# Kernel optimization log

Measured on AMD Instinct MI355X. Metric: run time of the kernel, lower is better.

Reference implementation:

```python
import jax, jax.numpy as jnp
import numpy as np

E, CIN, COUT, K = 8, 256, 256, 3
STRIDE, PAD, DIL, GROUPS = 1, 1, 1, 1
N, H, W = 32, 56, 56


def setup_inputs() -> dict:
    key = jax.random.key(0)
    k1, k2, k3 = jax.random.split(key, 3)
    x = jax.random.normal(k1, (N, CIN, H, W), jnp.float32)
    # expert weight bank: (E*COUT, CIN//GROUPS, K, K), as in the torch module
    weight = jax.random.normal(k2, (E * COUT, CIN // GROUPS, K, K), jnp.float32) * 0.05
    fc_w = jax.random.normal(k3, (E, CIN), jnp.float32) * 0.02
    fc_b = jnp.zeros((E,), jnp.float32)
    return {"x": x, "weight": weight, "fc_w": fc_w, "fc_b": fc_b}


def reference(x, weight, fc_w, fc_b):
    n = x.shape[0]
    # sigmoid gate from global-avg-pooled features: (n, E)
    gate = jax.nn.sigmoid(x.mean((2, 3)) @ fc_w.T + fc_b)
    # mix expert weights per sample: (n, COUT, CIN//GROUPS, K, K)
    w = (gate @ weight.reshape(E, -1)).reshape(n, COUT, CIN // GROUPS, K, K)

    def conv1(xi, wi):
        # xi: (CIN, H, W), wi: (COUT, CIN//GROUPS, K, K)
        return jax.lax.conv_general_dilated(
            xi[None], wi,
            window_strides=(STRIDE, STRIDE),
            padding=[(PAD, PAD), (PAD, PAD)],
            rhs_dilation=(DIL, DIL),
            feature_group_count=GROUPS,
            dimension_numbers=("NCHW", "OIHW", "NCHW"),
        )[0]

    return jax.vmap(conv1)(x, w)  # (n, COUT, H_out, W_out)
```

## Files before the change

kernel.cpp:

```cpp
#include <hip/hip_runtime.h>
#include <hip/hip_bf16.h>

#define E_    8
#define CIN_  256
#define COUT_ 256
#define NK    9
#define KTOT  2304
#define IMGH  56
#define IMGW  56
#define HW    3136
#define NBATCH 32
#define PADW  58
#define PADHW 3364

typedef __attribute__((ext_vector_type(8))) __bf16 bf16x8;
typedef __attribute__((ext_vector_type(4))) float f32x4;
typedef unsigned int u32;

__device__ __forceinline__ void gld_lds16(const __bf16* g, __bf16* l) {
    __builtin_amdgcn_global_load_lds(
        (const __attribute__((address_space(1))) void*)(g),
        (__attribute__((address_space(3))) void*)(l), 16, 0, 0);
}

__global__ __launch_bounds__(256) void halo_zero_kernel(__bf16* xTp) {
    const int total = NBATCH * 228 * 128;
    u32* p = (u32*)xTp;
    for (int idx = blockIdx.x * 256 + threadIdx.x; idx < total; idx += gridDim.x * 256) {
        const int n  = idx / (228 * 128);
        const int r  = idx - n * (228 * 128);
        const int hp = r >> 7;
        const int cp = r & 127;
        int px;
        if (hp < 58)       px = hp;
        else if (hp < 116) px = 57 * PADW + (hp - 58);
        else if (hp < 172) px = (hp - 116 + 1) * PADW;
        else               px = (hp - 172 + 1) * PADW + 57;
        p[((size_t)(n * PADHW + px)) * 128 + cp] = 0u;
    }
}

__global__ __launch_bounds__(256) void transpose_kernel(const float* __restrict__ x,
                                                        __bf16* __restrict__ xTp,
                                                        float* __restrict__ pooled) {
    __shared__ __bf16 t[64][66];
    const int px0 = blockIdx.x * 64;
    const int c0  = blockIdx.y * 64;
    const int n   = blockIdx.z;
    const int tid = threadIdx.x;
    {
        const int px_l = tid & 63;
        const int cb   = (tid >> 6) * 16;
        #pragma unroll
        for (int i = 0; i < 16; ++i) {
            const int cin_l = cb + i;
            t[cin_l][px_l] =
                (__bf16)x[((size_t)(n * CIN_ + c0 + cin_l)) * HW + px0 + px_l];
        }
    }
    __syncthreads();
    {
        const int cin_l = tid & 63;
        const int pb    = (tid >> 6) * 16;
        float s = 0.f;
        #pragma unroll
        for (int i = 0; i < 16; ++i) {
            const int px = px0 + pb + i;
            const int h  = px / IMGW;
            const int w  = px - h * IMGW;
            const __bf16 v = t[cin_l][pb + i];
            s += (float)v;
            xTp[((size_t)(n * PADHW + (h + 1) * PADW + (w + 1))) * CIN_ + c0 + cin_l] = v;
        }
        atomicAdd(&pooled[n * CIN_ + c0 + cin_l], s);
    }
}

__global__ __launch_bounds__(256) void gate_kernel(const float* __restrict__ pooled,
                                                   const float* __restrict__ fc_w,
                                                   const float* __restrict__ fc_b,
                                                   float* __restrict__ gate) {
    const int t = threadIdx.x;
    const int n = t >> 3, e = t & 7;
    const float* pv = pooled + n * CIN_;
    const float* wv = fc_w + e * CIN_;
    float s = 0.f;
    for (int c = 0; c < CIN_; ++c) s += pv[c] * wv[c];
    s = s * (1.0f / HW) + fc_b[e];
    gate[t] = 1.0f / (1.0f + expf(-s));
}

__global__ __launch_bounds__(256) void mix_kernel(const float* __restrict__ weight,
                                                  const float* __restrict__ gate,
                                                  __bf16* __restrict__ wmix) {
    __shared__ float wstage[KTOT];
    __shared__ __bf16 tlds[KTOT];
    const int cout = blockIdx.x;
    const int tid  = threadIdx.x;
    float wreg[E_][NK];
    for (int e = 0; e < E_; ++e) {
        const float* wp = weight + (size_t)(e * COUT_ + cout) * KTOT;
        #pragma unroll
        for (int i = 0; i < NK; ++i) wstage[tid + i * 256] = wp[tid + i * 256];
        __syncthreads();
        #pragma unroll
        for (int kk = 0; kk < NK; ++kk) wreg[e][kk] = wstage[tid * NK + kk];
        __syncthreads();
    }
    for (int n = 0; n < NBATCH; ++n) {
        float g[E_];
        #pragma unroll
        for (int e = 0; e < E_; ++e) g[e] = gate[n * E_ + e];
        float acc[NK];
        #pragma unroll
        for (int kk = 0; kk < NK; ++kk) acc[kk] = 0.f;
        #pragma unroll
        for (int e = 0; e < E_; ++e)
            #pragma unroll
            for (int kk = 0; kk < NK; ++kk) acc[kk] += g[e] * wreg[e][kk];
        #pragma unroll
        for (int kk = 0; kk < NK; ++kk) tlds[kk * 256 + tid] = (__bf16)acc[kk];
        __syncthreads();
        u32* dst = (u32*)(wmix + ((size_t)(n * COUT_ + cout)) * KTOT);
        const u32* src = (const u32*)tlds;
        #pragma unroll
        for (int j = 0; j < 4; ++j) dst[tid + j * 256] = src[tid + j * 256];
        if (tid < 128) dst[tid + 1024] = src[tid + 1024];
        __syncthreads();
    }
}

#define BM 256
#define BN 224

__global__ __launch_bounds__(512) void conv_kernel(const __bf16* __restrict__ xTp,
                                                   const __bf16* __restrict__ wmix,
                                                   float* __restrict__ out) {
    __shared__ __attribute__((aligned(16))) __bf16 At[2][BM * 64];
    __shared__ __attribute__((aligned(16))) __bf16 Bt[2][BN * 64];

    const int bid = blockIdx.x;
    const int swz = (bid & 7) * 56 + (bid >> 3);
    const int n   = swz / 14;
    const int pt  = swz - n * 14;
    const int p0  = pt * BN;

    const int tid  = threadIdx.x;
    const int lane = tid & 63;
    const int wave = tid >> 6;
    const int lr   = lane >> 3;
    const int sl   = lane & 7;
    const int swzsl = sl ^ lr;

    const __bf16* wmixn = wmix + (size_t)n * COUT_ * KTOT;
    const __bf16* xTpn  = xTp + (size_t)n * PADHW * CIN_;

    const __bf16* asrc[4];
    #pragma unroll
    for (int i = 0; i < 4; ++i) {
        const int j = wave + 8 * i;
        asrc[i] = wmixn + (size_t)(8 * j + lr) * KTOT + swzsl * 8;
    }
    const __bf16* bsrc[4];
    #pragma unroll
    for (int i = 0; i < 4; ++i) {
        int j = wave + 8 * i; if (j > 27) j = 27;
        const int px = p0 + 8 * j + lr;
        const int h  = px / IMGW;
        const int w  = px - h * IMGW;
        bsrc[i] = xTpn + (size_t)(h * PADW + w) * CIN_ + swzsl * 8;
    }

    const f32x4 zero = {0.f, 0.f, 0.f, 0.f};
    f32x4 acc[4][7];
    #pragma unroll
    for (int i = 0; i < 4; ++i)
        #pragma unroll
        for (int j = 0; j < 7; ++j) acc[i][j] = zero;

    const int mbase = (wave >> 1) * 64;
    const int nbase = (wave & 1) * 112;
    const int fr = lane & 15;
    const int kg = lane >> 4;
    const int fswz = fr & 7;

    auto STAGE = [&](int buf, int stepk, int toff) {
        #pragma unroll
        for (int i = 0; i < 4; ++i)
            gld_lds16(asrc[i] + stepk * 64, &At[buf][(wave + 8 * i) * 512]);
        const int boff = toff * 256 + (stepk & 3) * 64;
        #pragma unroll
        for (int i = 0; i < 4; ++i)
            if (wave < 4 || i < 3)
                gld_lds16(bsrc[i] + boff, &Bt[buf][(wave + 8 * i) * 512]);
    };

    auto COMPUTE = [&](const __bf16* Ab, const __bf16* Bb) {
        #pragma unroll
        for (int ks = 0; ks < 2; ++ks) {
            const int soff = ((ks * 4 + kg) ^ fswz) * 8;
            bf16x8 a[4], b[7];
            #pragma unroll
            for (int m = 0; m < 4; ++m)
                a[m] = *(const bf16x8*)(Ab + (mbase + m * 16 + fr) * 64 + soff);
            #pragma unroll
            for (int nn = 0; nn < 7; ++nn)
                b[nn] = *(const bf16x8*)(Bb + (nbase + nn * 16 + fr) * 64 + soff);
            #pragma unroll
            for (int m = 0; m < 4; ++m)
                #pragma unroll
                for (int nn = 0; nn < 7; ++nn)
                    acc[m][nn] = __builtin_amdgcn_mfma_f32_16x16x32_bf16(
                        a[m], b[nn], acc[m][nn], 0, 0, 0);
        }
    };

    STAGE(0, 0, 0);
    __syncthreads();
    for (int khw = 0; khw < 9; ++khw) {
        const int kh  = (khw * 11) >> 5;
        const int kw  = khw - kh * 3;
        const int toff = kh * PADW + kw;
        const int kh2 = ((khw + 1) * 11) >> 5;
        const int kw2 = (khw + 1) - kh2 * 3;
        const int toff2 = kh2 * PADW + kw2;
        #pragma unroll
        for (int cb = 0; cb < 4; ++cb) {
            const int buf  = cb & 1;
            const int step = khw * 4 + cb;
            if (step < 35)
                STAGE(buf ^ 1, step + 1, (cb < 3) ? toff : toff2);
            COMPUTE(&At[buf][0], &Bt[buf][0]);
            __syncthreads();
        }
    }

    const int rbase = kg * 4;
    #pragma unroll
    for (int m = 0; m < 4; ++m)
        #pragma unroll
        for (int nn = 0; nn < 7; ++nn) {
            float* op = out + (size_t)(n * COUT_ + mbase + m * 16 + rbase) * HW
                            + p0 + nbase + nn * 16 + fr;
            #pragma unroll
            for (int r = 0; r < 4; ++r)
                op[(size_t)r * HW] = acc[m][nn][r];
        }
}

extern "C" void kernel_launch(void* const* d_in, const int* in_sizes, int n_in,
                              void* d_out, int out_size, void* d_ws, size_t ws_size,
                              hipStream_t stream) {
    const float* x      = (const float*)d_in[0];
    const float* weight = (const float*)d_in[1];
    const float* fc_w   = (const float*)d_in[2];
    const float* fc_b   = (const float*)d_in[3];
    float* out = (float*)d_out;

    char* ws = (char*)d_ws;
    float* pooled = (float*)ws;
    float* gate   = (float*)(ws + 32 * 1024);
    __bf16* wmix  = (__bf16*)(ws + 64 * 1024);
    __bf16* xTp   = (__bf16*)(ws + 64 * 1024 +
                              (size_t)NBATCH * COUT_ * KTOT * 2);

    hipMemsetAsync(pooled, 0, NBATCH * CIN_ * sizeof(float), stream);
    halo_zero_kernel<<<dim3(512), 256, 0, stream>>>(xTp);
    transpose_kernel<<<dim3(49, 4, NBATCH), 256, 0, stream>>>(x, xTp, pooled);
    gate_kernel<<<dim3(1), 256, 0, stream>>>(pooled, fc_w, fc_b, gate);
    mix_kernel<<<dim3(COUT_), 256, 0, stream>>>(weight, gate, wmix);
    conv_kernel<<<dim3(448), 512, 0, stream>>>(xTp, wmix, out);
}
```

Baseline: 199.5 us.

## Restructure conv main loop with staged MFMA phases and split mix kernel

The conv kernel's double-buffered loop is replaced by a pipeline that keeps two stages in flight, waiting on vmcnt instead of a full __syncthreads. Each K-step is split into phases that load LDS fragments and then issue MFMAs at raised priority between explicit barriers, so waves interleave. Separately, the memset is folded into the halo-zero kernel to drop a launch, and mix_kernel gains a batch dimension in its grid to expose more parallelism. The B staging now loads all four slots with a clamped index, where before it skipped the redundant one, which adds some duplicate loads. The extra barriers could also add synchronisation cost.

```diff
diff --git a/kernel.cpp b/kernel.cpp
--- a/kernel.cpp
+++ b/kernel.cpp
@@ -23,10 +23,12 @@
         (__attribute__((address_space(3))) void*)(l), 16, 0, 0);
 }
 
-__global__ __launch_bounds__(256) void halo_zero_kernel(__bf16* xTp) {
+__global__ __launch_bounds__(256) void init_kernel(__bf16* xTp, float* pooled) {
+    const int tid0 = blockIdx.x * 256 + threadIdx.x;
+    if (tid0 < NBATCH * CIN_) pooled[tid0] = 0.f;
     const int total = NBATCH * 228 * 128;
     u32* p = (u32*)xTp;
-    for (int idx = blockIdx.x * 256 + threadIdx.x; idx < total; idx += gridDim.x * 256) {
+    for (int idx = tid0; idx < total; idx += gridDim.x * 256) {
         const int n  = idx / (228 * 128);
         const int r  = idx - n * (228 * 128);
         const int hp = r >> 7;
@@ -96,6 +98,7 @@
     __shared__ float wstage[KTOT];
     __shared__ __bf16 tlds[KTOT];
     const int cout = blockIdx.x;
+    const int n0   = blockIdx.y * 8;
     const int tid  = threadIdx.x;
     float wreg[E_][NK];
     for (int e = 0; e < E_; ++e) {
@@ -107,7 +110,7 @@
         for (int kk = 0; kk < NK; ++kk) wreg[e][kk] = wstage[tid * NK + kk];
         __syncthreads();
     }
-    for (int n = 0; n < NBATCH; ++n) {
+    for (int n = n0; n < n0 + 8; ++n) {
         float g[E_];
         #pragma unroll
         for (int e = 0; e < E_; ++e) g[e] = gate[n * E_ + e];
@@ -162,9 +165,11 @@
         asrc[i] = wmixn + (size_t)(8 * j + lr) * KTOT + swzsl * 8;
     }
     const __bf16* bsrc[4];
+    int bj[4];
     #pragma unroll
     for (int i = 0; i < 4; ++i) {
         int j = wave + 8 * i; if (j > 27) j = 27;
+        bj[i] = j;
         const int px = p0 + 8 * j + lr;
         const int h  = px / IMGW;
         const int w  = px - h * IMGW;
@@ -184,56 +189,115 @@
     const int kg = lane >> 4;
     const int fswz = fr & 7;
 
-    auto STAGE = [&](int buf, int stepk, int toff) {
+    auto STAGE = [&](int buf, int step) {
+        const int khw  = step >> 2;
+        const int kh   = (khw * 11) >> 5;
+        const int kw   = khw - kh * 3;
+        const int aoff = step * 64;
+        const int boff = (kh * PADW + kw) * 256 + (step & 3) * 64;
         #pragma unroll
         for (int i = 0; i < 4; ++i)
-            gld_lds16(asrc[i] + stepk * 64, &At[buf][(wave + 8 * i) * 512]);
-        const int boff = toff * 256 + (stepk & 3) * 64;
+            gld_lds16(asrc[i] + aoff, &At[buf][(wave + 8 * i) * 512]);
         #pragma unroll
         for (int i = 0; i < 4; ++i)
-            if (wave < 4 || i < 3)
-                gld_lds16(bsrc[i] + boff, &Bt[buf][(wave + 8 * i) * 512]);
+            gld_lds16(bsrc[i] + boff, &Bt[buf][bj[i] * 512]);
     };
 
-    auto COMPUTE = [&](const __bf16* Ab, const __bf16* Bb) {
+    auto TILE = [&](int buf) {
+        const __bf16* Ab = &At[buf][0];
+        const __bf16* Bb = &Bt[buf][0];
+        bf16x8 a0[2], a1[2], a2[2], a3[2], bA[2], bB[2];
         #pragma unroll
         for (int ks = 0; ks < 2; ++ks) {
-            const int soff = ((ks * 4 + kg) ^ fswz) * 8;
-            bf16x8 a[4], b[7];
+            const int so = ((ks * 4 + kg) ^ fswz) * 8;
+            a0[ks] = *(const bf16x8*)(Ab + (mbase +      fr) * 64 + so);
+            a1[ks] = *(const bf16x8*)(Ab + (mbase + 16 + fr) * 64 + so);
+            a2[ks] = *(const bf16x8*)(Ab + (mbase + 32 + fr) * 64 + so);
+            a3[ks] = *(const bf16x8*)(Ab + (mbase + 48 + fr) * 64 + so);
+            bA[ks] = *(const bf16x8*)(Bb + (nbase +      fr) * 64 + so);
+            bB[ks] = *(const bf16x8*)(Bb + (nbase + 16 + fr) * 64 + so);
+        }
+        __builtin_amdgcn_s_barrier();
+        asm volatile("s_waitcnt lgkmcnt(0)" ::: "memory");
+        __builtin_amdgcn_sched_barrier(0);
+        __builtin_amdgcn_s_setprio(1);
+        #pragma unroll
+        for (int ks = 0; ks < 2; ++ks) {
+            acc[0][0] = __builtin_amdgcn_mfma_f32_16x16x32_bf16(a0[ks], bA[ks], acc[0][0], 0, 0, 0);
+            acc[1][0] = __builtin_amdgcn_mfma_f32_16x16x32_bf16(a1[ks], bA[ks], acc[1][0], 0, 0, 0);
+            acc[2][0] = __builtin_amdgcn_mfma_f32_16x16x32_bf16(a2[ks], bA[ks], acc[2][0], 0, 0, 0);
+            acc[3][0] = __builtin_amdgcn_mfma_f32_16x16x32_bf16(a3[ks], bA[ks], acc[3][0], 0, 0, 0);
+            acc[0][1] = __builtin_amdgcn_mfma_f32_16x16x32_bf16(a0[ks], bB[ks], acc[0][1], 0, 0, 0);
+            acc[1][1] = __builtin_amdgcn_mfma_f32_16x16x32_bf16(a1[ks], bB[ks], acc[1][1], 0, 0, 0);
+            acc[2][1] = __builtin_amdgcn_mfma_f32_16x16x32_bf16(a2[ks], bB[ks], acc[2][1], 0, 0, 0);
+            acc[3][1] = __builtin_amdgcn_mfma_f32_16x16x32_bf16(a3[ks], bB[ks], acc[3][1], 0, 0, 0);
+        }
+        __builtin_amdgcn_s_setprio(0);
+        __builtin_amdgcn_sched_barrier(0);
+        __builtin_amdgcn_s_barrier();
+        #pragma unroll
+        for (int q = 1; q < 3; ++q) {
+            const int nb = nbase + q * 32;
             #pragma unroll
-            for (int m = 0; m < 4; ++m)
-                a[m] = *(const bf16x8*)(Ab + (mbase + m * 16 + fr) * 64 + soff);
+            for (int ks = 0; ks < 2; ++ks) {
+                const int so = ((ks * 4 + kg) ^ fswz) * 8;
+                bA[ks] = *(const bf16x8*)(Bb + (nb +      fr) * 64 + so);
+                bB[ks] = *(const bf16x8*)(Bb + (nb + 16 + fr) * 64 + so);
+            }
+            __builtin_amdgcn_s_barrier();
+            asm volatile("s_waitcnt lgkmcnt(0)" ::: "memory");
+            __builtin_amdgcn_sched_barrier(0);
+            __builtin_amdgcn_s_setprio(1);
             #pragma unroll
-            for (int nn = 0; nn < 7; ++nn)
-                b[nn] = *(const bf16x8*)(Bb + (nbase + nn * 16 + fr) * 64 + soff);
-            #pragma unroll
-            for (int m = 0; m < 4; ++m)
-                #pragma unroll
-                for (int nn = 0; nn < 7; ++nn)
-                    acc[m][nn] = __builtin_amdgcn_mfma_f32_16x16x32_bf16(
-                        a[m], b[nn], acc[m][nn], 0, 0, 0);
-        }
+            for (int ks = 0; ks < 2; ++ks) {
+                acc[0][2*q]   = __builtin_amdgcn_mfma_f32_16x16x32_bf16(a0[ks], bA[ks], acc[0][2*q],   0, 0, 0);
+                acc[1][2*q]   = __builtin_amdgcn_mfma_f32_16x16x32_bf16(a1[ks], bA[ks], acc[1][2*q],   0, 0, 0);
+                acc[2][2*q]   = __builtin_amdgcn_mfma_f32_16x16x32_bf16(a2[ks], bA[ks], acc[2][2*q],   0, 0, 0);
+                acc[3][2*q]   = __builtin_amdgcn_mfma_f32_16x16x32_bf16(a3[ks], bA[ks], acc[3][2*q],   0, 0, 0);
+                acc[0][2*q+1] = __builtin_amdgcn_mfma_f32_16x16x32_bf16(a0[ks], bB[ks], acc[0][2*q+1], 0, 0, 0);
+                acc[1][2*q+1] = __builtin_amdgcn_mfma_f32_16x16x32_bf16(a1[ks], bB[ks], acc[1][2*q+1], 0, 0, 0);
+                acc[2][2*q+1] = __builtin_amdgcn_mfma_f32_16x16x32_bf16(a2[ks], bB[ks], acc[2][2*q+1], 0, 0, 0);
+                acc[3][2*q+1] = __builtin_amdgcn_mfma_f32_16x16x32_bf16(a3[ks], bB[ks], acc[3][2*q+1], 0, 0, 0);
+            }
+            __builtin_amdgcn_s_setprio(0);
+            __builtin_amdgcn_sched_barrier(0);
+            __builtin_amdgcn_s_barrier();
+        }
+        #pragma unroll
+        for (int ks = 0; ks < 2; ++ks) {
+            const int so = ((ks * 4 + kg) ^ fswz) * 8;
+            bA[ks] = *(const bf16x8*)(Bb + (nbase + 96 + fr) * 64 + so);
+        }
+        __builtin_amdgcn_s_barrier();
+        asm volatile("s_waitcnt lgkmcnt(0)" ::: "memory");
+        __builtin_amdgcn_sched_barrier(0);
+        __builtin_amdgcn_s_setprio(1);
+        #pragma unroll
+        for (int ks = 0; ks < 2; ++ks) {
+            acc[0][6] = __builtin_amdgcn_mfma_f32_16x16x32_bf16(a0[ks], bA[ks], acc[0][6], 0, 0, 0);
+            acc[1][6] = __builtin_amdgcn_mfma_f32_16x16x32_bf16(a1[ks], bA[ks], acc[1][6], 0, 0, 0);
+            acc[2][6] = __builtin_amdgcn_mfma_f32_16x16x32_bf16(a2[ks], bA[ks], acc[2][6], 0, 0, 0);
+            acc[3][6] = __builtin_amdgcn_mfma_f32_16x16x32_bf16(a3[ks], bA[ks], acc[3][6], 0, 0, 0);
+        }
+        __builtin_amdgcn_s_setprio(0);
+        __builtin_amdgcn_sched_barrier(0);
+        __builtin_amdgcn_s_barrier();
     };
 
-    STAGE(0, 0, 0);
-    __syncthreads();
-    for (int khw = 0; khw < 9; ++khw) {
-        const int kh  = (khw * 11) >> 5;
-        const int kw  = khw - kh * 3;
-        const int toff = kh * PADW + kw;
-        const int kh2 = ((khw + 1) * 11) >> 5;
-        const int kw2 = (khw + 1) - kh2 * 3;
-        const int toff2 = kh2 * PADW + kw2;
-        #pragma unroll
-        for (int cb = 0; cb < 4; ++cb) {
-            const int buf  = cb & 1;
-            const int step = khw * 4 + cb;
-            if (step < 35)
-                STAGE(buf ^ 1, step + 1, (cb < 3) ? toff : toff2);
-            COMPUTE(&At[buf][0], &Bt[buf][0]);
-            __syncthreads();
-        }
-    }
+    STAGE(0, 0);
+    STAGE(1, 1);
+    for (int t = 0; t < 35; ++t) {
+        const int buf = t & 1;
+        asm volatile("s_waitcnt vmcnt(8)" ::: "memory");
+        __builtin_amdgcn_s_barrier();
+        __builtin_amdgcn_sched_barrier(0);
+        TILE(buf);
+        if (t + 2 < 36) STAGE(buf, t + 2);
+    }
+    asm volatile("s_waitcnt vmcnt(0)" ::: "memory");
+    __builtin_amdgcn_s_barrier();
+    __builtin_amdgcn_sched_barrier(0);
+    TILE(1);
 
     const int rbase = kg * 4;
     #pragma unroll
@@ -264,10 +328,9 @@
     __bf16* xTp   = (__bf16*)(ws + 64 * 1024 +
                               (size_t)NBATCH * COUT_ * KTOT * 2);
 
-    hipMemsetAsync(pooled, 0, NBATCH * CIN_ * sizeof(float), stream);
-    halo_zero_kernel<<<dim3(512), 256, 0, stream>>>(xTp);
+    init_kernel<<<dim3(512), 256, 0, stream>>>(xTp, pooled);
     transpose_kernel<<<dim3(49, 4, NBATCH), 256, 0, stream>>>(x, xTp, pooled);
     gate_kernel<<<dim3(1), 256, 0, stream>>>(pooled, fc_w, fc_b, gate);
-    mix_kernel<<<dim3(COUT_), 256, 0, stream>>>(weight, gate, wmix);
+    mix_kernel<<<dim3(COUT_, 4), 256, 0, stream>>>(weight, gate, wmix);
     conv_kernel<<<dim3(448), 512, 0, stream>>>(xTp, wmix, out);
 }
```

Result: slower. 222.0 us (+11.3%).

## Deepen conv prefetch pipeline, split mix kernel over batch, fuse pooled memset

Applied to the files above, without the earlier changes.

The conv main loop is restructured into a flat 36-step loop. It keeps two stages in flight, waits with an explicit vmcnt and uses raw s_barrier with sched_barriers, aiming to overlap global-to-LDS loads with MFMA compute better. The mix kernel's grid is split four ways over the batch for more parallelism, though each block now reloads its expert weights. The pooled memset is folded into the halo-zero kernel to drop one launch. The B staging now has every wave issue all four loads, with redundant loads clamped to row 27, which adds some duplicate load traffic.

```diff
diff --git a/kernel.cpp b/kernel.cpp
--- a/kernel.cpp
+++ b/kernel.cpp
@@ -23,10 +23,12 @@
         (__attribute__((address_space(3))) void*)(l), 16, 0, 0);
 }
 
-__global__ __launch_bounds__(256) void halo_zero_kernel(__bf16* xTp) {
+__global__ __launch_bounds__(256) void init_kernel(__bf16* xTp, float* pooled) {
+    const int tid0 = blockIdx.x * 256 + threadIdx.x;
+    if (tid0 < NBATCH * CIN_) pooled[tid0] = 0.f;
     const int total = NBATCH * 228 * 128;
     u32* p = (u32*)xTp;
-    for (int idx = blockIdx.x * 256 + threadIdx.x; idx < total; idx += gridDim.x * 256) {
+    for (int idx = tid0; idx < total; idx += gridDim.x * 256) {
         const int n  = idx / (228 * 128);
         const int r  = idx - n * (228 * 128);
         const int hp = r >> 7;
@@ -96,6 +98,7 @@
     __shared__ float wstage[KTOT];
     __shared__ __bf16 tlds[KTOT];
     const int cout = blockIdx.x;
+    const int n0   = blockIdx.y * 8;
     const int tid  = threadIdx.x;
     float wreg[E_][NK];
     for (int e = 0; e < E_; ++e) {
@@ -107,7 +110,7 @@
         for (int kk = 0; kk < NK; ++kk) wreg[e][kk] = wstage[tid * NK + kk];
         __syncthreads();
     }
-    for (int n = 0; n < NBATCH; ++n) {
+    for (int n = n0; n < n0 + 8; ++n) {
         float g[E_];
         #pragma unroll
         for (int e = 0; e < E_; ++e) g[e] = gate[n * E_ + e];
@@ -162,9 +165,11 @@
         asrc[i] = wmixn + (size_t)(8 * j + lr) * KTOT + swzsl * 8;
     }
     const __bf16* bsrc[4];
+    int bj[4];
     #pragma unroll
     for (int i = 0; i < 4; ++i) {
         int j = wave + 8 * i; if (j > 27) j = 27;
+        bj[i] = j;
         const int px = p0 + 8 * j + lr;
         const int h  = px / IMGW;
         const int w  = px - h * IMGW;
@@ -184,15 +189,18 @@
     const int kg = lane >> 4;
     const int fswz = fr & 7;
 
-    auto STAGE = [&](int buf, int stepk, int toff) {
+    auto STAGE = [&](int buf, int step) {
+        const int khw  = step >> 2;
+        const int kh   = (khw * 11) >> 5;
+        const int kw   = khw - kh * 3;
+        const int aoff = step * 64;
+        const int boff = (kh * PADW + kw) * 256 + (step & 3) * 64;
         #pragma unroll
         for (int i = 0; i < 4; ++i)
-            gld_lds16(asrc[i] + stepk * 64, &At[buf][(wave + 8 * i) * 512]);
-        const int boff = toff * 256 + (stepk & 3) * 64;
+            gld_lds16(asrc[i] + aoff, &At[buf][(wave + 8 * i) * 512]);
         #pragma unroll
         for (int i = 0; i < 4; ++i)
-            if (wave < 4 || i < 3)
-                gld_lds16(bsrc[i] + boff, &Bt[buf][(wave + 8 * i) * 512]);
+            gld_lds16(bsrc[i] + boff, &Bt[buf][bj[i] * 512]);
     };
 
     auto COMPUTE = [&](const __bf16* Ab, const __bf16* Bb) {
@@ -215,25 +223,23 @@
         }
     };
 
-    STAGE(0, 0, 0);
-    __syncthreads();
-    for (int khw = 0; khw < 9; ++khw) {
-        const int kh  = (khw * 11) >> 5;
-        const int kw  = khw - kh * 3;
-        const int toff = kh * PADW + kw;
-        const int kh2 = ((khw + 1) * 11) >> 5;
-        const int kw2 = (khw + 1) - kh2 * 3;
-        const int toff2 = kh2 * PADW + kw2;
-        #pragma unroll
-        for (int cb = 0; cb < 4; ++cb) {
-            const int buf  = cb & 1;
-            const int step = khw * 4 + cb;
-            if (step < 35)
-                STAGE(buf ^ 1, step + 1, (cb < 3) ? toff : toff2);
-            COMPUTE(&At[buf][0], &Bt[buf][0]);
-            __syncthreads();
-        }
-    }
+    STAGE(0, 0);
+    STAGE(1, 1);
+    for (int t = 0; t < 35; ++t) {
+        const int buf = t & 1;
+        asm volatile("s_waitcnt vmcnt(8)" ::: "memory");
+        __builtin_amdgcn_s_barrier();
+        __builtin_amdgcn_sched_barrier(0);
+        COMPUTE(&At[buf][0], &Bt[buf][0]);
+        __builtin_amdgcn_sched_barrier(0);
+        __builtin_amdgcn_s_barrier();
+        __builtin_amdgcn_sched_barrier(0);
+        if (t + 2 < 36) STAGE(buf, t + 2);
+    }
+    asm volatile("s_waitcnt vmcnt(0)" ::: "memory");
+    __builtin_amdgcn_s_barrier();
+    __builtin_amdgcn_sched_barrier(0);
+    COMPUTE(&At[1][0], &Bt[1][0]);
 
     const int rbase = kg * 4;
     #pragma unroll
@@ -264,10 +270,9 @@
     __bf16* xTp   = (__bf16*)(ws + 64 * 1024 +
                               (size_t)NBATCH * COUT_ * KTOT * 2);
 
-    hipMemsetAsync(pooled, 0, NBATCH * CIN_ * sizeof(float), stream);
-    halo_zero_kernel<<<dim3(512), 256, 0, stream>>>(xTp);
+    init_kernel<<<dim3(512), 256, 0, stream>>>(xTp, pooled);
     transpose_kernel<<<dim3(49, 4, NBATCH), 256, 0, stream>>>(x, xTp, pooled);
     gate_kernel<<<dim3(1), 256, 0, stream>>>(pooled, fc_w, fc_b, gate);
-    mix_kernel<<<dim3(COUT_), 256, 0, stream>>>(weight, gate, wmix);
+    mix_kernel<<<dim3(COUT_, 4), 256, 0, stream>>>(weight, gate, wmix);
     conv_kernel<<<dim3(448), 512, 0, stream>>>(xTp, wmix, out);
 }
```

Result: no change. 203.1 us (+1.8%).
